# Kernel optimization log

Hardware: AMD Instinct MI355X
Metric: run time of the kernel (lower is better)

The kernel has to match this reference:

```python
import jax, jax.numpy as jnp
import numpy as np

IN_DIM = 64  # channels; theta/phi -> C//8, g -> C//2


def _maxpool2x2(t):
    # t: [B, c, H, W] -> [B, c, H//2, W//2]
    B, c, H, W = t.shape
    return t.reshape(B, c, H // 2, 2, W // 2, 2).max(axis=(3, 5))


def setup_inputs() -> dict:
    key = jax.random.key(0)
    ks = jax.random.split(key, 6)
    C = IN_DIM
    x = jax.random.normal(ks[0], (16, C, 64, 64), dtype=jnp.float32)
    # 1x1 convs stored as [out, in] matrices (kernel is 1x1, no bias)
    w_theta = jax.random.normal(ks[1], (C // 8, C), dtype=jnp.float32) * (1.0 / np.sqrt(C))
    w_phi = jax.random.normal(ks[2], (C // 8, C), dtype=jnp.float32) * (1.0 / np.sqrt(C))
    w_g = jax.random.normal(ks[3], (C // 2, C), dtype=jnp.float32) * (1.0 / np.sqrt(C))
    w_o = jax.random.normal(ks[4], (C, C // 2), dtype=jnp.float32) * (1.0 / np.sqrt(C // 2))
    gamma = jax.random.normal(ks[5], (), dtype=jnp.float32)  # torch inits to 0; nonzero for testing
    return {"x": x, "w_theta": w_theta, "w_phi": w_phi, "w_g": w_g, "w_o": w_o, "gamma": gamma}


def reference(x, w_theta, w_phi, w_g, w_o, gamma):
    B, C, H, W = x.shape
    # 1x1 conv projections (pointwise channel matmuls)
    theta = jnp.einsum('oc,bchw->bohw', w_theta, x).reshape(B, C // 8, H * W)
    phi = _maxpool2x2(jnp.einsum('oc,bchw->bohw', w_phi, x)).reshape(B, C // 8, H * W // 4)
    g = _maxpool2x2(jnp.einsum('oc,bchw->bohw', w_g, x)).reshape(B, C // 2, H * W // 4)
    # attention: [B, HW, HW/4]
    beta = jax.nn.softmax(jnp.einsum('bcn,bcm->bnm', theta, phi), axis=-1)
    # aggregate values: g @ beta^T -> [B, C//2, HW]
    o = jnp.einsum('bcm,bnm->bcn', g, beta).reshape(B, C // 2, H, W)
    o = jnp.einsum('oc,bchw->bohw', w_o, o)
    return gamma * o + x
```

## Files before the change

### kernel.cpp

```cpp
#include <hip/hip_runtime.h>

typedef _Float16 half4v __attribute__((ext_vector_type(4)));
typedef float    float4v __attribute__((ext_vector_type(4)));

#define BB 16
#define CC 64
#define NN 4096
#define MM 1024
#define LN256 5.545177444479562f

static __device__ __forceinline__ float4v mfma16(half4v a, half4v b, float4v c) {
    return __builtin_amdgcn_mfma_f32_16x16x16f16(a, b, c, 0, 0, 0);
}

__device__ __forceinline__ unsigned pk2(float a, float b) {
    union { _Float16 h[2]; unsigned u; } cv;
    cv.h[0] = (_Float16)a; cv.h[1] = (_Float16)b;
    return cv.u;
}

__global__ __launch_bounds__(128, 4) void proj_kernel(
    const float* __restrict__ x,
    const float* __restrict__ w_th,
    const float* __restrict__ w_ph,
    const float* __restrict__ w_g,
    _Float16* __restrict__ theta,
    _Float16* __restrict__ phi,
    _Float16* __restrict__ gT)
{
    __shared__ float wlds[64 * 32];

    const int b   = blockIdx.y;
    const int blk = blockIdx.x;
    const int z   = blockIdx.z;
    const int t   = threadIdx.x;

    if (z == 0) {
        for (int i = t; i < 1024; i += 128) {
            int c = i >> 4, o = i & 15;
            wlds[i] = (o < 8) ? w_th[o * 64 + c] : w_ph[(o - 8) * 64 + c];
        }
    } else {
        for (int i = t; i < 2048; i += 128) {
            int c = i >> 5, o = i & 31;
            wlds[i] = w_g[o * 64 + c];
        }
    }
    __syncthreads();

    const float2* x2 = (const float2*)(x + (size_t)b * CC * NN);
    const int p2 = blk * 128 + t;
    const int l = t & 63, w = t >> 6;
    const int m = (blk * 2 + w) * 32 + (l & 31);

    if (z == 0) {
        float th0[8], th1[8], ph0[8], ph1[8];
#pragma unroll
        for (int i = 0; i < 8; i++) { th0[i]=th1[i]=ph0[i]=ph1[i]=0.f; }
#pragma unroll 4
        for (int c = 0; c < 64; c++) {
            float2 xv = x2[c * (NN / 2) + p2];
            const float4* w4 = (const float4*)&wlds[c * 16];
            float4 wv[4];
#pragma unroll
            for (int j = 0; j < 4; j++) wv[j] = w4[j];
            const float* wf = (const float*)wv;
#pragma unroll
            for (int o = 0; o < 8; o++) {
                th0[o] = fmaf(wf[o], xv.x, th0[o]);
                th1[o] = fmaf(wf[o], xv.y, th1[o]);
                ph0[o] = fmaf(wf[8 + o], xv.x, ph0[o]);
                ph1[o] = fmaf(wf[8 + o], xv.y, ph1[o]);
            }
        }
        uint4* tw = (uint4*)(theta + ((size_t)b * NN + 2 * p2) * 8);
        tw[0] = make_uint4(pk2(th0[0],th0[1]), pk2(th0[2],th0[3]),
                           pk2(th0[4],th0[5]), pk2(th0[6],th0[7]));
        tw[1] = make_uint4(pk2(th1[0],th1[1]), pk2(th1[2],th1[3]),
                           pk2(th1[4],th1[5]), pk2(th1[6],th1[7]));
        float phm[8];
#pragma unroll
        for (int i = 0; i < 8; i++) phm[i] = fmaxf(ph0[i], ph1[i]);
#pragma unroll
        for (int i = 0; i < 8; i++) phm[i] = fmaxf(phm[i], __shfl_xor(phm[i], 32));
        if (l < 32) {
            uint4* pw = (uint4*)(phi + ((size_t)b * MM + m) * 8);
            pw[0] = make_uint4(pk2(phm[0],phm[1]), pk2(phm[2],phm[3]),
                               pk2(phm[4],phm[5]), pk2(phm[6],phm[7]));
        }
    } else {
        float gg0[32], gg1[32];
#pragma unroll
        for (int i = 0; i < 32; i++) { gg0[i] = gg1[i] = 0.f; }
#pragma unroll 4
        for (int c = 0; c < 64; c++) {
            float2 xv = x2[c * (NN / 2) + p2];
            const float4* w4 = (const float4*)&wlds[c * 32];
            float4 wv[8];
#pragma unroll
            for (int j = 0; j < 8; j++) wv[j] = w4[j];
            const float* wf = (const float*)wv;
#pragma unroll
            for (int o = 0; o < 32; o++) {
                gg0[o] = fmaf(wf[o], xv.x, gg0[o]);
                gg1[o] = fmaf(wf[o], xv.y, gg1[o]);
            }
        }
        float ggm[32];
#pragma unroll
        for (int i = 0; i < 32; i++) ggm[i] = fmaxf(gg0[i], gg1[i]);
#pragma unroll
        for (int i = 0; i < 32; i++) ggm[i] = fmaxf(ggm[i], __shfl_xor(ggm[i], 32));
        const int cofs = (l < 32) ? 0 : 16;
        _Float16* gp = gT + ((size_t)b * 32 + cofs) * MM + m;
#pragma unroll
        for (int c2 = 0; c2 < 16; c2++)
            gp[(size_t)c2 * MM] = (_Float16)ggm[cofs + c2];
    }
}

__global__ __launch_bounds__(256, 4) void attn_kernel(
    const _Float16* __restrict__ theta,
    const _Float16* __restrict__ phi,
    const _Float16* __restrict__ gT,
    const float* __restrict__ w_o,
    const float* __restrict__ gamma_p,
    const float* __restrict__ x,
    float* __restrict__ out)
{
    __shared__ __align__(16) _Float16 phl[128 * 24];
    __shared__ __align__(16) _Float16 gl[32 * 136];

    const int b    = blockIdx.y;
    const int t    = threadIdx.x;
    const int wave = t >> 6;
    const int lane = t & 63;
    const int col  = lane & 15;
    const int q    = lane >> 4;
    const int nbase = blockIdx.x * 64 + wave * 16;

    const float4v zero4 = {0.f, 0.f, 0.f, 0.f};

    if (t < 128)
        *(float4*)&phl[t * 24 + 8] = make_float4(0.f, 0.f, 0.f, 0.f);

    half4v thB = (half4v){0, 0, 0, 0};
    if (q < 2)
        thB = *(const half4v*)(theta + ((size_t)b * NN + nbase + col) * 8 + q * 4);

    half4v onesA = (half4v){0, 0, 0, 0};
    if (col == 0) {
        onesA[0] = (_Float16)1; onesA[1] = (_Float16)1;
        onesA[2] = (_Float16)1; onesA[3] = (_Float16)1;
    }

    float mx = -1e30f;
    for (int m0 = 0; m0 < MM; m0 += 128) {
        __syncthreads();
        if (t < 128)
            *(float4*)&phl[t * 24] =
                *(const float4*)(phi + ((size_t)b * MM + m0 + t) * 8);
        __syncthreads();
#pragma unroll
        for (int mt = 0; mt < 8; mt++) {
            half4v af = *(const half4v*)&phl[(mt * 16 + col) * 24 + q * 4];
            float4v S = mfma16(af, thB, zero4);
            mx = fmaxf(mx, fmaxf(fmaxf(S.x, S.y), fmaxf(S.z, S.w)));
        }
    }
    mx = fmaxf(mx, __shfl_xor(mx, 16));
    mx = fmaxf(mx, __shfl_xor(mx, 32));
    const float shift = mx - LN256;

    float4v acc0 = zero4, acc1 = zero4, accd = zero4;

    for (int m0 = 0; m0 < MM; m0 += 128) {
        __syncthreads();
        if (t < 128)
            *(float4*)&phl[t * 24] =
                *(const float4*)(phi + ((size_t)b * MM + m0 + t) * 8);
        {
            int c = t >> 3, seg = (t & 7) * 16;
            const _Float16* src = gT + ((size_t)b * 32 + c) * MM + m0 + seg;
            float4 v0 = *(const float4*)src;
            float4 v1 = *(const float4*)(src + 8);
            *(float4*)&gl[c * 136 + seg]     = v0;
            *(float4*)&gl[c * 136 + seg + 8] = v1;
        }
        __syncthreads();

#pragma unroll 2
        for (int mt = 0; mt < 8; mt++) {
            half4v af = *(const half4v*)&phl[(mt * 16 + col) * 24 + q * 4];
            float4v S = mfma16(af, thB, zero4);
            half4v P;
            P[0] = (_Float16)__expf(S.x - shift);
            P[1] = (_Float16)__expf(S.y - shift);
            P[2] = (_Float16)__expf(S.z - shift);
            P[3] = (_Float16)__expf(S.w - shift);
            half4v ag0 = *(const half4v*)&gl[col * 136 + mt * 16 + q * 4];
            half4v ag1 = *(const half4v*)&gl[(col + 16) * 136 + mt * 16 + q * 4];
            acc0 = mfma16(ag0, P, acc0);
            acc1 = mfma16(ag1, P, acc1);
            accd = mfma16(onesA, P, accd);
        }
    }

    float dv = __shfl(accd.x, col);
    float sc = gamma_p[0] / dv;

    half4v B0, B1;
    B0[0] = (_Float16)(acc0.x * sc); B0[1] = (_Float16)(acc0.y * sc);
    B0[2] = (_Float16)(acc0.z * sc); B0[3] = (_Float16)(acc0.w * sc);
    B1[0] = (_Float16)(acc1.x * sc); B1[1] = (_Float16)(acc1.y * sc);
    B1[2] = (_Float16)(acc1.z * sc); B1[3] = (_Float16)(acc1.w * sc);

#pragma unroll
    for (int ct = 0; ct < 4; ct++) {
        const float* wp = w_o + (size_t)(ct * 16 + col) * 32 + q * 4;
        float4 w0 = *(const float4*)wp;
        float4 w1 = *(const float4*)(wp + 16);
        half4v wa, wb;
        wa[0] = (_Float16)w0.x; wa[1] = (_Float16)w0.y;
        wa[2] = (_Float16)w0.z; wa[3] = (_Float16)w0.w;
        wb[0] = (_Float16)w1.x; wb[1] = (_Float16)w1.y;
        wb[2] = (_Float16)w1.z; wb[3] = (_Float16)w1.w;
        float4v D = mfma16(wa, B0, zero4);
        D = mfma16(wb, B1, D);
#pragma unroll
        for (int r = 0; r < 4; r++) {
            int co = ct * 16 + q * 4 + r;
            size_t idx = ((size_t)b * CC + co) * NN + nbase + col;
            out[idx] = D[r] + x[idx];
        }
    }
}

extern "C" void kernel_launch(void* const* d_in, const int* in_sizes, int n_in,
                              void* d_out, int out_size, void* d_ws, size_t ws_size,
                              hipStream_t stream) {
    const float* x       = (const float*)d_in[0];
    const float* w_theta = (const float*)d_in[1];
    const float* w_phi   = (const float*)d_in[2];
    const float* w_g     = (const float*)d_in[3];
    const float* w_o     = (const float*)d_in[4];
    const float* gamma   = (const float*)d_in[5];
    float* out = (float*)d_out;

    _Float16* theta_ws = (_Float16*)d_ws;
    _Float16* phi_ws   = theta_ws + (size_t)BB * NN * 8;
    _Float16* gT_ws    = phi_ws   + (size_t)BB * MM * 8;

    proj_kernel<<<dim3(16, BB, 2), 128, 0, stream>>>(
        x, w_theta, w_phi, w_g, theta_ws, phi_ws, gT_ws);

    attn_kernel<<<dim3(NN / 64, BB), 256, 0, stream>>>(
        theta_ws, phi_ws, gT_ws, w_o, gamma, x, out);
}
```

Measured before the change: 123.5 us.

## Stage full phi once in LDS and compute g projection in packed fp16

The attention kernel now loads the entire per-batch phi tensor (1024x8 fp16) into LDS once, instead of reloading 128-row chunks with barriers in both the max pass and the accumulation pass. This removes repeated global loads and extra syncs, and masks lanes q>=2 to zero instead of relying on padding. Separately, the g projection in proj_kernel uses packed fp16 FMAs with fp16 weights in LDS, halving register and LDS footprint but accumulating in half precision, which adds rounding risk.

```diff
diff --git a/kernel.cpp b/kernel.cpp
--- a/kernel.cpp
+++ b/kernel.cpp
@@ -1,6 +1,7 @@
 #include <hip/hip_runtime.h>
 
 typedef _Float16 half4v __attribute__((ext_vector_type(4)));
+typedef _Float16 h2     __attribute__((ext_vector_type(2)));
 typedef float    float4v __attribute__((ext_vector_type(4)));
 
 #define BB 16
@@ -17,6 +18,19 @@
     union { _Float16 h[2]; unsigned u; } cv;
     cv.h[0] = (_Float16)a; cv.h[1] = (_Float16)b;
     return cv.u;
+}
+__device__ __forceinline__ h2 ash2(unsigned u) {
+    union { unsigned u; h2 h; } c; c.u = u; return c.h;
+}
+__device__ __forceinline__ h2 hmax2(h2 a, h2 b) {
+    h2 r;
+    r.x = (a.x > b.x) ? a.x : b.x;
+    r.y = (a.y > b.y) ? a.y : b.y;
+    return r;
+}
+__device__ __forceinline__ h2 shfl_xor_h2(h2 v, int m) {
+    union { h2 h; int i; } c; c.h = v; c.i = __shfl_xor(c.i, m);
+    return c.h;
 }
 
 __global__ __launch_bounds__(128, 4) void proj_kernel(
@@ -28,7 +42,8 @@
     _Float16* __restrict__ phi,
     _Float16* __restrict__ gT)
 {
-    __shared__ float wlds[64 * 32];
+    __shared__ __align__(16) float wlds[64 * 16];
+    unsigned* wl2 = (unsigned*)wlds;
 
     const int b   = blockIdx.y;
     const int blk = blockIdx.x;
@@ -41,9 +56,9 @@
             wlds[i] = (o < 8) ? w_th[o * 64 + c] : w_ph[(o - 8) * 64 + c];
         }
     } else {
-        for (int i = t; i < 2048; i += 128) {
-            int c = i >> 5, o = i & 31;
-            wlds[i] = w_g[o * 64 + c];
+        for (int i = t; i < 1024; i += 128) {
+            int c = i >> 4, o2 = i & 15;
+            wl2[i] = pk2(w_g[(2 * o2) * 64 + c], w_g[(2 * o2 + 1) * 64 + c]);
         }
     }
     __syncthreads();
@@ -89,33 +104,38 @@
                                pk2(phm[4],phm[5]), pk2(phm[6],phm[7]));
         }
     } else {
-        float gg0[32], gg1[32];
-#pragma unroll
-        for (int i = 0; i < 32; i++) { gg0[i] = gg1[i] = 0.f; }
+        h2 ga[16], gb[16];
+#pragma unroll
+        for (int i = 0; i < 16; i++) { ga[i] = (h2)0; gb[i] = (h2)0; }
 #pragma unroll 4
         for (int c = 0; c < 64; c++) {
             float2 xv = x2[c * (NN / 2) + p2];
-            const float4* w4 = (const float4*)&wlds[c * 32];
-            float4 wv[8];
-#pragma unroll
-            for (int j = 0; j < 8; j++) wv[j] = w4[j];
-            const float* wf = (const float*)wv;
-#pragma unroll
-            for (int o = 0; o < 32; o++) {
-                gg0[o] = fmaf(wf[o], xv.x, gg0[o]);
-                gg1[o] = fmaf(wf[o], xv.y, gg1[o]);
+            const uint4* w4 = (const uint4*)&wl2[c * 16];
+            uint4 q0 = w4[0], q1 = w4[1], q2 = w4[2], q3 = w4[3];
+            unsigned wv[16] = {q0.x,q0.y,q0.z,q0.w, q1.x,q1.y,q1.z,q1.w,
+                               q2.x,q2.y,q2.z,q2.w, q3.x,q3.y,q3.z,q3.w};
+            _Float16 hx = (_Float16)xv.x, hy = (_Float16)xv.y;
+            h2 xa; xa.x = hx; xa.y = hx;
+            h2 xb; xb.x = hy; xb.y = hy;
+#pragma unroll
+            for (int k = 0; k < 16; k++) {
+                ga[k] = __builtin_elementwise_fma(ash2(wv[k]), xa, ga[k]);
+                gb[k] = __builtin_elementwise_fma(ash2(wv[k]), xb, gb[k]);
             }
         }
-        float ggm[32];
-#pragma unroll
-        for (int i = 0; i < 32; i++) ggm[i] = fmaxf(gg0[i], gg1[i]);
-#pragma unroll
-        for (int i = 0; i < 32; i++) ggm[i] = fmaxf(ggm[i], __shfl_xor(ggm[i], 32));
-        const int cofs = (l < 32) ? 0 : 16;
-        _Float16* gp = gT + ((size_t)b * 32 + cofs) * MM + m;
-#pragma unroll
-        for (int c2 = 0; c2 < 16; c2++)
-            gp[(size_t)c2 * MM] = (_Float16)ggm[cofs + c2];
+        h2 gm[16];
+#pragma unroll
+        for (int k = 0; k < 16; k++) gm[k] = hmax2(ga[k], gb[k]);
+#pragma unroll
+        for (int k = 0; k < 16; k++) gm[k] = hmax2(gm[k], shfl_xor_h2(gm[k], 32));
+        const int k0 = (l < 32) ? 0 : 8;
+        _Float16* gp = gT + ((size_t)b * 32 + 2 * k0) * MM + m;
+#pragma unroll
+        for (int k = 0; k < 8; k++) {
+            h2 v = gm[k0 + k];
+            gp[(size_t)(2 * k) * MM]     = v.x;
+            gp[(size_t)(2 * k + 1) * MM] = v.y;
+        }
     }
 }
 
@@ -128,7 +148,7 @@
     const float* __restrict__ x,
     float* __restrict__ out)
 {
-    __shared__ __align__(16) _Float16 phl[128 * 24];
+    __shared__ __align__(16) _Float16 phl[MM * 8];
     __shared__ __align__(16) _Float16 gl[32 * 136];
 
     const int b    = blockIdx.y;
@@ -140,33 +160,35 @@
     const int nbase = blockIdx.x * 64 + wave * 16;
 
     const float4v zero4 = {0.f, 0.f, 0.f, 0.f};
-
-    if (t < 128)
-        *(float4*)&phl[t * 24 + 8] = make_float4(0.f, 0.f, 0.f, 0.f);
-
-    half4v thB = (half4v){0, 0, 0, 0};
+    const half4v zeroh = {0, 0, 0, 0};
+
+    {
+        const float4* src = (const float4*)(phi + (size_t)b * MM * 8);
+        float4* dst = (float4*)phl;
+#pragma unroll
+        for (int i = 0; i < 4; i++) dst[t + i * 256] = src[t + i * 256];
+    }
+
+    half4v thB = zeroh;
     if (q < 2)
         thB = *(const half4v*)(theta + ((size_t)b * NN + nbase + col) * 8 + q * 4);
 
-    half4v onesA = (half4v){0, 0, 0, 0};
+    half4v onesA = zeroh;
     if (col == 0) {
         onesA[0] = (_Float16)1; onesA[1] = (_Float16)1;
         onesA[2] = (_Float16)1; onesA[3] = (_Float16)1;
     }
 
+    __syncthreads();
+
     float mx = -1e30f;
-    for (int m0 = 0; m0 < MM; m0 += 128) {
-        __syncthreads();
-        if (t < 128)
-            *(float4*)&phl[t * 24] =
-                *(const float4*)(phi + ((size_t)b * MM + m0 + t) * 8);
-        __syncthreads();
-#pragma unroll
-        for (int mt = 0; mt < 8; mt++) {
-            half4v af = *(const half4v*)&phl[(mt * 16 + col) * 24 + q * 4];
-            float4v S = mfma16(af, thB, zero4);
-            mx = fmaxf(mx, fmaxf(fmaxf(S.x, S.y), fmaxf(S.z, S.w)));
-        }
+#pragma unroll 4
+    for (int mt = 0; mt < 64; mt++) {
+        half4v af = zeroh;
+        if (q < 2)
+            af = *(const half4v*)&phl[(mt * 16 + col) * 8 + q * 4];
+        float4v S = mfma16(af, thB, zero4);
+        mx = fmaxf(mx, fmaxf(fmaxf(S.x, S.y), fmaxf(S.z, S.w)));
     }
     mx = fmaxf(mx, __shfl_xor(mx, 16));
     mx = fmaxf(mx, __shfl_xor(mx, 32));
@@ -176,9 +198,6 @@
 
     for (int m0 = 0; m0 < MM; m0 += 128) {
         __syncthreads();
-        if (t < 128)
-            *(float4*)&phl[t * 24] =
-                *(const float4*)(phi + ((size_t)b * MM + m0 + t) * 8);
         {
             int c = t >> 3, seg = (t & 7) * 16;
             const _Float16* src = gT + ((size_t)b * 32 + c) * MM + m0 + seg;
@@ -191,7 +210,9 @@
 
 #pragma unroll 2
         for (int mt = 0; mt < 8; mt++) {
-            half4v af = *(const half4v*)&phl[(mt * 16 + col) * 24 + q * 4];
+            half4v af = zeroh;
+            if (q < 2)
+                af = *(const half4v*)&phl[(m0 + mt * 16 + col) * 8 + q * 4];
             float4v S = mfma16(af, thB, zero4);
             half4v P;
             P[0] = (_Float16)__expf(S.x - shift);
```

After: 118.7 us. 1.04x faster.
